# Optimization experiments

Measured on AMD Instinct MI355X. Metric: run time of the kernel, lower is better.

## Reference

```python
import jax, jax.numpy as jnp
import numpy as np

B, D, H, O = 32, 128, 256, 10


def setup_inputs() -> dict:
    key = jax.random.key(0)
    ks = jax.random.split(key, 8)
    return {
        "t": jax.random.uniform(ks[0], (1,), dtype=jnp.float32),
        "state_batch": jax.random.normal(ks[1], (2 * B, D), dtype=jnp.float32),
        "x0": jax.random.normal(ks[2], (B, D), dtype=jnp.float32),
        "x1": jax.random.normal(ks[3], (B, D), dtype=jnp.float32),
        "W1": jax.random.normal(ks[4], (D, H), dtype=jnp.float32) / np.sqrt(D),
        "b1": jax.random.normal(ks[5], (H,), dtype=jnp.float32) * 0.01,
        "W2": jax.random.normal(ks[6], (H, O), dtype=jnp.float32) / np.sqrt(H),
        "b2": jax.random.normal(ks[7], (O,), dtype=jnp.float32) * 0.01,
    }


def reference(t, state_batch, x0, x1, W1, b1, W2, b2):
    b = x0.shape[0]
    deviation, dev_velocity = state_batch[:b], state_batch[b:]  # [B,D] each
    tt = t[0]
    window = 4.0 * tt * (1.0 - tt)
    # point on the perturbed path
    x = x0 + tt * (x1 - x0) + window * deviation  # [B,D]

    def f_single(xs):  # [D] -> [O]
        return jnp.tanh(xs @ W1 + b1) @ W2 + b2

    def G_single(xs):  # [D] -> [D,D] pullback metric J^T J + eps I
        J = jax.jacrev(f_single)(xs)  # [O,D] (O small -> reverse mode)
        return J.T @ J + 1e-4 * jnp.eye(xs.shape[0], dtype=xs.dtype)

    # dG[b,i,j,k] = d G_ij / d x_k  -- replaces the torch double autograd loop
    dG = jax.vmap(jax.jacfwd(G_single))(x)  # [B,D,D,D]
    dG = dG / (jnp.sqrt(jnp.sum(dG * dG, axis=(1, 2, 3), keepdims=True)) + 1e-6)
    # Christoffel symbols (first kind, up to normalization as in source)
    Gamma = 0.5 * (dG + jnp.transpose(dG, (0, 2, 1, 3)) - jnp.transpose(dG, (0, 3, 1, 2)))
    a = -jnp.einsum('bijk,bj,bk->bi', Gamma, dev_velocity, dev_velocity)
    a = a / (jnp.linalg.norm(dev_velocity, axis=1, keepdims=True) + 1e-6)
    restoration = -0.1 * deviation
    return jnp.concatenate([dev_velocity, a + restoration], axis=0)  # [2B,D]
```

## Files before the change

kernel.cpp:

```cpp
#include <hip/hip_runtime.h>
#include <hip/hip_bf16.h>


#define NB 32

#define OP    0
#define OE    65536
#define OCW   163840
#define OAUN  245760
#define OVN   249856

template<int BF> __device__ __forceinline__ float ld(const void* p, int i) {
  if constexpr (BF) return __bfloat162float(((const __hip_bfloat16*)p)[i]);
  else return ((const float*)p)[i];
}
template<int BF> __device__ __forceinline__ void st(void* p, int i, float v) {
  if constexpr (BF) ((__hip_bfloat16*)p)[i] = __float2bfloat16(v);
  else ((float*)p)[i] = v;
}

__device__ __forceinline__ int blocksniff(const void* sb, int* sh) {
  if (threadIdx.x == 0) *sh = 0;
  __syncthreads();
  float v = fabsf(__bfloat162float(((const __hip_bfloat16*)sb)[threadIdx.x & 255]));
  if (!(v < 1000.0f)) atomicOr(sh, 1);
  __syncthreads();
  return (*sh == 0) ? 1 : 0;
}

#define LXS   0
#define LVS   128
#define LW2   256
#define LTMP  2816
#define LYS   3072
#define LSMV  3088
#define LSAR  3344
#define LF1   3600
#define LEL   5136
#define LCL   8208
#define LSW2  8320
#define LTOT  11392

template<int BF>
__device__ void k1_body(const void* tin, const void* sbin, const void* x0in,
                        const void* x1in, const void* W1in, const void* b1in,
                        const void* W2in, float* ws, float* sm) {
  int bid = blockIdx.x, t = threadIdx.x;
  if (bid < 256) {
    float* colh = sm;
    if (t < 128) colh[t] = ld<BF>(W1in, t * 256 + bid);
    __syncthreads();
    float pacc = 0.f;
    for (int d = 0; d < 128; d += 4) {
      float4 c4 = *(const float4*)&colh[d];
      pacc += c4.x * ld<BF>(W1in, (d + 0) * 256 + t);
      pacc += c4.y * ld<BF>(W1in, (d + 1) * 256 + t);
      pacc += c4.z * ld<BF>(W1in, (d + 2) * 256 + t);
      pacc += c4.w * ld<BF>(W1in, (d + 3) * 256 + t);
    }
    ws[OP + bid * 256 + t] = pacc;
    return;
  }
  int b = bid - 256;
  float tt = ld<BF>(tin, 0);
  float window = 4.f * tt * (1.f - tt);
  if (t < 128) {
    float dev = ld<BF>(sbin, b * 128 + t);
    float v   = ld<BF>(sbin, (NB + b) * 128 + t);
    float x0v = ld<BF>(x0in, b * 128 + t);
    float x1v = ld<BF>(x1in, b * 128 + t);
    sm[LXS + t] = x0v + tt * (x1v - x0v) + window * dev;
    sm[LVS + t] = v;
  }
  for (int i = t; i < 2560; i += 256) sm[LW2 + i] = ld<BF>(W2in, i);
  __syncthreads();
  float hacc = ld<BF>(b1in, t), wacc = 0.f;
  for (int d = 0; d < 128; ++d) {
    float w1v = ld<BF>(W1in, d * 256 + t);
    hacc += w1v * sm[LXS + d];
    wacc += w1v * sm[LVS + d];
  }
  float z  = tanhf(hacc);
  float sg = 1.f - z * z;
  float ug = -2.f * z * sg;
  sm[LSAR + t] = sg;
  sm[LTMP + t] = (t < 128) ? sm[LVS + t] * sm[LVS + t] : 0.f;
  __syncthreads();
  for (int off = 128; off > 0; off >>= 1) {
    if (t < off) sm[LTMP + t] += sm[LTMP + t + off];
    __syncthreads();
  }
  if (t == 0) ws[OVN + b] = sqrtf(sm[LTMP]);
  __syncthreads();
  sm[LTMP + t] = ug * wacc * wacc;
  __syncthreads();
  if (t < 10) {
    float y = 0.f;
    for (int h = 0; h < 256; ++h) y += sm[LW2 + h * 10 + t] * sm[LTMP + h];
    sm[LYS + t] = y;
  }
  __syncthreads();
  {
    float mg = 0.f;
    #pragma unroll
    for (int o = 0; o < 10; ++o) mg += sm[LW2 + t * 10 + o] * sm[LYS + o];
    sm[LSMV + t] = sg * mg;
  }
  for (int i = t; i < 3072; i += 256) {
    int g = i / 12, c = i % 12;
    sm[LSW2 + i] = (c < 10) ? sm[LSAR + g] * sm[LW2 + g * 10 + c] : 0.f;
  }
  __syncthreads();
  if (t < 128) {
    float a = 0.f;
    for (int g = 0; g < 256; ++g) a += ld<BF>(W1in, t * 256 + g) * sm[LSMV + g];
    ws[OAUN + b * 128 + t] = a;
  }
  if (t < 128) {
    float fa[10];
    #pragma unroll
    for (int o = 0; o < 10; ++o) fa[o] = 0.f;
    for (int g = 0; g < 256; ++g) {
      float w1v = ld<BF>(W1in, t * 256 + g);
      const float* sp = &sm[LSW2 + g * 12];
      float4 a0 = *(const float4*)sp;
      float4 a1 = *(const float4*)(sp + 4);
      float2 a2 = *(const float2*)(sp + 8);
      fa[0] += w1v * a0.x; fa[1] += w1v * a0.y; fa[2] += w1v * a0.z; fa[3] += w1v * a0.w;
      fa[4] += w1v * a1.x; fa[5] += w1v * a1.y; fa[6] += w1v * a1.z; fa[7] += w1v * a1.w;
      fa[8] += w1v * a2.x; fa[9] += w1v * a2.y;
    }
    #pragma unroll
    for (int o = 0; o < 10; ++o) sm[LF1 + t * 12 + o] = fa[o];
    sm[LF1 + t * 12 + 10] = 0.f; sm[LF1 + t * 12 + 11] = 0.f;
  }
  __syncthreads();
  float er[10];
  #pragma unroll
  for (int o = 0; o < 10; ++o) er[o] = 0.f;
  for (int d = 0; d < 128; ++d) {
    float w1v = ld<BF>(W1in, d * 256 + t);
    const float* fp = &sm[LF1 + d * 12];
    float4 a0 = *(const float4*)fp;
    float4 a1 = *(const float4*)(fp + 4);
    float2 a2 = *(const float2*)(fp + 8);
    er[0] += w1v * a0.x; er[1] += w1v * a0.y; er[2] += w1v * a0.z; er[3] += w1v * a0.w;
    er[4] += w1v * a1.x; er[5] += w1v * a1.y; er[6] += w1v * a1.z; er[7] += w1v * a1.w;
    er[8] += w1v * a2.x; er[9] += w1v * a2.y;
  }
  #pragma unroll
  for (int o = 0; o < 10; ++o) sm[LEL + t * 12 + o] = er[o];
  {
    float* gp = ws + OE + (b * 256 + t) * 12;
    *(float4*)gp       = make_float4(er[0], er[1], er[2], er[3]);
    *(float4*)(gp + 4) = make_float4(er[4], er[5], er[6], er[7]);
    *(float4*)(gp + 8) = make_float4(er[8], er[9], ug, 0.f);
  }
  __syncthreads();
  if (t < 100) {
    int o = t / 10, p = t % 10;
    float c = 0.f;
    for (int g = 0; g < 256; ++g)
      c += sm[LW2 + g * 10 + o] * sm[LSAR + g] * sm[LEL + g * 12 + p];
    sm[LCL + t] = c;
  }
  __syncthreads();
  {
    float w2r[10];
    #pragma unroll
    for (int p = 0; p < 10; ++p) w2r[p] = sm[LW2 + t * 10 + p];
    #pragma unroll
    for (int o = 0; o < 10; ++o) {
      float cw = 0.f;
      #pragma unroll
      for (int p = 0; p < 10; ++p) cw += sm[LCL + o * 10 + p] * w2r[p];
      ws[OCW + b * 2560 + o * 256 + t] = cw;
    }
  }
}

__global__ __launch_bounds__(256) void K1(const void* tin, const void* sbin,
                                          const void* x0in, const void* x1in,
                                          const void* W1in, const void* b1in,
                                          const void* W2in, float* ws) {
  __shared__ int sh;
  __shared__ __align__(16) float sm[LTOT];
  int bf = blocksniff(sbin, &sh);
  if (bf) k1_body<1>(tin, sbin, x0in, x1in, W1in, b1in, W2in, ws, sm);
  else    k1_body<0>(tin, sbin, x0in, x1in, W1in, b1in, W2in, ws, sm);
}

template<int BF>
__device__ void k2_body(const void* sbin, const void* W2in, void* out, float* ws,
                        float* rec, float* w2h, float* red) {
  int b = blockIdx.x, t = threadIdx.x;
  int w = t >> 6;
  for (int i = t; i < 3072; i += 256) rec[i] = ws[OE + b * 3072 + i];
  for (int i = t; i < 3072; i += 256) {
    int r = i / 12, c = i % 12;
    w2h[i] = (c < 10) ? ld<BF>(W2in, r * 10 + c) : 0.f;
  }
  __syncthreads();
  float cwr[10], er[10], w2r[10];
  #pragma unroll
  for (int o = 0; o < 10; ++o) cwr[o] = ws[OCW + b * 2560 + o * 256 + t];
  #pragma unroll
  for (int o = 0; o < 10; ++o) er[o] = rec[t * 12 + o];
  float uT = rec[t * 12 + 10];
  #pragma unroll
  for (int o = 0; o < 10; ++o) w2r[o] = w2h[t * 12 + o];
  float acc = 0.f;
  for (int i = 0; i < 64; ++i) {
    int h = w * 64 + i;
    float Ph = ws[OP + h * 256 + t];
    const float* rp = &rec[h * 12];
    float4 E0 = *(const float4*)rp;
    float4 E1 = *(const float4*)(rp + 4);
    float4 E2 = *(const float4*)(rp + 8);
    const float* wp = &w2h[h * 12];
    float4 W0 = *(const float4*)wp;
    float4 W1v = *(const float4*)(wp + 4);
    float4 W2v = *(const float4*)(wp + 8);
    float R = E0.x*w2r[0] + E0.y*w2r[1] + E0.z*w2r[2] + E0.w*w2r[3]
            + E1.x*w2r[4] + E1.y*w2r[5] + E1.z*w2r[6] + E1.w*w2r[7]
            + E2.x*w2r[8] + E2.y*w2r[9];
    float Rt = W0.x*er[0] + W0.y*er[1] + W0.z*er[2] + W0.w*er[3]
             + W1v.x*er[4] + W1v.y*er[5] + W1v.z*er[6] + W1v.w*er[7]
             + W2v.x*er[8] + W2v.y*er[9];
    float Qd = W0.x*cwr[0] + W0.y*cwr[1] + W0.z*cwr[2] + W0.w*cwr[3]
             + W1v.x*cwr[4] + W1v.y*cwr[5] + W1v.z*cwr[6] + W1v.w*cwr[7]
             + W2v.x*cwr[8] + W2v.y*cwr[9];
    acc += E2.z * Ph * (Ph * Qd + R * Rt);
  }
  red[t] = acc * uT;
  __syncthreads();
  for (int off = 128; off > 0; off >>= 1) {
    if (t < off) red[t] += red[t + off];
    __syncthreads();
  }
  float F = sqrtf(fmaxf(2.f * red[0], 0.f));
  float denom = (F + 1e-6f) * (ws[OVN + b] + 1e-6f);
  if (t < 128) {
    st<BF>(out, b * 128 + t, ld<BF>(sbin, (NB + b) * 128 + t));
    float dev = ld<BF>(sbin, b * 128 + t);
    float val = -ws[OAUN + b * 128 + t] / denom - 0.1f * dev;
    st<BF>(out, (NB + b) * 128 + t, val);
  }
}

__global__ __launch_bounds__(256) void K2(const void* sbin, const void* W2in,
                                          void* out, float* ws) {
  __shared__ int sh;
  __shared__ __align__(16) float rec[3072];
  __shared__ __align__(16) float w2h[3072];
  __shared__ float red[256];
  int bf = blocksniff(sbin, &sh);
  if (bf) k2_body<1>(sbin, W2in, out, ws, rec, w2h, red);
  else    k2_body<0>(sbin, W2in, out, ws, rec, w2h, red);
}

extern "C" void kernel_launch(void* const* d_in, const int* in_sizes, int n_in,
                              void* d_out, int out_size, void* d_ws, size_t ws_size,
                              hipStream_t stream) {
  float* ws = (float*)d_ws;
  const void* tin  = d_in[0];
  const void* sbin = d_in[1];
  const void* x0in = d_in[2];
  const void* x1in = d_in[3];
  const void* W1in = d_in[4];
  const void* b1in = d_in[5];
  const void* W2in = d_in[6];

  K1<<<dim3(288), dim3(256), 0, stream>>>(tin, sbin, x0in, x1in, W1in, b1in, W2in, ws);
  K2<<<dim3(32),  dim3(256), 0, stream>>>(sbin, W2in, d_out, ws);
}
```

Before: 113.4 us.

## Restructure K1/K2 reductions with wave shuffles and split F1 across all threads

The per-batch blocks in K1 now run first, ahead of the P-matrix blocks. The ys and vnorm reductions use wave shuffles instead of shared-memory tree reductions. The a_un matvec is derived algebraically from F1 and ys rather than a separate 256-long dot per thread, and the F1 and C computations are split across both thread halves with vectorized W1 loads. K2 uses float4 copies, batches P loads eight at a time, and replaces its tree reduction with a shuffle reduction. The aim is to cut serial reduction depth, barrier count and redundant W1 reads, at the cost of a slightly different floating-point summation order.

```diff
diff --git a/kernel.cpp b/kernel.cpp
--- a/kernel.cpp
+++ b/kernel.cpp
@@ -18,6 +18,17 @@
   if constexpr (BF) ((__hip_bfloat16*)p)[i] = __float2bfloat16(v);
   else ((float*)p)[i] = v;
 }
+__device__ __forceinline__ float b2f(unsigned short u) {
+  return __uint_as_float(((unsigned int)u) << 16);
+}
+template<int BF> __device__ __forceinline__ float4 ld4(const void* p, int i) {
+  if constexpr (BF) {
+    ushort4 u = *(const ushort4*)((const unsigned short*)p + i);
+    return make_float4(b2f(u.x), b2f(u.y), b2f(u.z), b2f(u.w));
+  } else {
+    return *(const float4*)((const float*)p + i);
+  }
+}
 
 __device__ __forceinline__ int blocksniff(const void* sb, int* sh) {
   if (threadIdx.x == 0) *sh = 0;
@@ -31,24 +42,34 @@
 #define LXS   0
 #define LVS   128
 #define LW2   256
-#define LTMP  2816
-#define LYS   3072
-#define LSMV  3088
-#define LSAR  3344
-#define LF1   3600
-#define LEL   5136
-#define LCL   8208
-#define LSW2  8320
-#define LTOT  11392
+#define LYS   2816
+#define LRED  2832
+#define LF1   2880
+#define LEL   4416
+#define LSW2  7488
+#define LCL   10560
+#define LCL2  10660
+#define LTOT  10760
+
+#define F1ACC(wv, gidx) do { \
+    const float* sp_ = &sm[LSW2 + (gidx)*12]; \
+    float4 s0_ = *(const float4*)sp_; \
+    float4 s1_ = *(const float4*)(sp_+4); \
+    float2 s2_ = *(const float2*)(sp_+8); \
+    fa[0]+=(wv)*s0_.x; fa[1]+=(wv)*s0_.y; fa[2]+=(wv)*s0_.z; fa[3]+=(wv)*s0_.w; \
+    fa[4]+=(wv)*s1_.x; fa[5]+=(wv)*s1_.y; fa[6]+=(wv)*s1_.z; fa[7]+=(wv)*s1_.w; \
+    fa[8]+=(wv)*s2_.x; fa[9]+=(wv)*s2_.y; \
+  } while (0)
 
 template<int BF>
 __device__ void k1_body(const void* tin, const void* sbin, const void* x0in,
                         const void* x1in, const void* W1in, const void* b1in,
                         const void* W2in, float* ws, float* sm) {
   int bid = blockIdx.x, t = threadIdx.x;
-  if (bid < 256) {
+  if (bid >= NB) {
+    int row = bid - NB;
     float* colh = sm;
-    if (t < 128) colh[t] = ld<BF>(W1in, t * 256 + bid);
+    if (t < 128) colh[t] = ld<BF>(W1in, t * 256 + row);
     __syncthreads();
     float pacc = 0.f;
     for (int d = 0; d < 128; d += 4) {
@@ -58,10 +79,11 @@
       pacc += c4.z * ld<BF>(W1in, (d + 2) * 256 + t);
       pacc += c4.w * ld<BF>(W1in, (d + 3) * 256 + t);
     }
-    ws[OP + bid * 256 + t] = pacc;
+    ws[OP + row * 256 + t] = pacc;
     return;
   }
-  int b = bid - 256;
+  int b = bid;
+  int w = t >> 6;
   float tt = ld<BF>(tin, 0);
   float window = 4.f * tt * (1.f - tt);
   if (t < 128) {
@@ -75,64 +97,71 @@
   for (int i = t; i < 2560; i += 256) sm[LW2 + i] = ld<BF>(W2in, i);
   __syncthreads();
   float hacc = ld<BF>(b1in, t), wacc = 0.f;
-  for (int d = 0; d < 128; ++d) {
-    float w1v = ld<BF>(W1in, d * 256 + t);
-    hacc += w1v * sm[LXS + d];
-    wacc += w1v * sm[LVS + d];
+  for (int d = 0; d < 128; d += 4) {
+    float4 xv = *(const float4*)&sm[LXS + d];
+    float4 vv = *(const float4*)&sm[LVS + d];
+    float w0 = ld<BF>(W1in, (d + 0) * 256 + t);
+    float w1 = ld<BF>(W1in, (d + 1) * 256 + t);
+    float w2 = ld<BF>(W1in, (d + 2) * 256 + t);
+    float w3 = ld<BF>(W1in, (d + 3) * 256 + t);
+    hacc += w0 * xv.x + w1 * xv.y + w2 * xv.z + w3 * xv.w;
+    wacc += w0 * vv.x + w1 * vv.y + w2 * vv.z + w3 * vv.w;
   }
   float z  = tanhf(hacc);
   float sg = 1.f - z * z;
   float ug = -2.f * z * sg;
-  sm[LSAR + t] = sg;
-  sm[LTMP + t] = (t < 128) ? sm[LVS + t] * sm[LVS + t] : 0.f;
-  __syncthreads();
-  for (int off = 128; off > 0; off >>= 1) {
-    if (t < off) sm[LTMP + t] += sm[LTMP + t + off];
-    __syncthreads();
-  }
-  if (t == 0) ws[OVN + b] = sqrtf(sm[LTMP]);
-  __syncthreads();
-  sm[LTMP + t] = ug * wacc * wacc;
-  __syncthreads();
-  if (t < 10) {
-    float y = 0.f;
-    for (int h = 0; h < 256; ++h) y += sm[LW2 + h * 10 + t] * sm[LTMP + h];
-    sm[LYS + t] = y;
-  }
-  __syncthreads();
+  float w2r[10];
+  #pragma unroll
+  for (int o = 0; o < 10; ++o) w2r[o] = sm[LW2 + t * 10 + o];
+  #pragma unroll
+  for (int o = 0; o < 10; ++o) sm[LSW2 + t * 12 + o] = sg * w2r[o];
+  float cval = ug * wacc * wacc;
+  float rv[11];
+  #pragma unroll
+  for (int o = 0; o < 10; ++o) rv[o] = cval * w2r[o];
+  rv[10] = (t < 128) ? sm[LVS + t] * sm[LVS + t] : 0.f;
+  #pragma unroll
+  for (int o = 0; o < 11; ++o) {
+    float v = rv[o];
+    #pragma unroll
+    for (int m = 32; m > 0; m >>= 1) v += __shfl_xor(v, m);
+    if ((t & 63) == 0) sm[LRED + w * 12 + o] = v;
+  }
+  __syncthreads();
+  if (t < 11) {
+    float s = sm[LRED + t] + sm[LRED + 12 + t] + sm[LRED + 24 + t] + sm[LRED + 36 + t];
+    if (t < 10) sm[LYS + t] = s;
+    else        ws[OVN + b] = sqrtf(s);
+  }
+  int half = t >> 7, r = t & 127;
+  float fa[10];
+  #pragma unroll
+  for (int o = 0; o < 10; ++o) fa[o] = 0.f;
   {
-    float mg = 0.f;
-    #pragma unroll
-    for (int o = 0; o < 10; ++o) mg += sm[LW2 + t * 10 + o] * sm[LYS + o];
-    sm[LSMV + t] = sg * mg;
-  }
-  for (int i = t; i < 3072; i += 256) {
-    int g = i / 12, c = i % 12;
-    sm[LSW2 + i] = (c < 10) ? sm[LSAR + g] * sm[LW2 + g * 10 + c] : 0.f;
-  }
-  __syncthreads();
-  if (t < 128) {
-    float a = 0.f;
-    for (int g = 0; g < 256; ++g) a += ld<BF>(W1in, t * 256 + g) * sm[LSMV + g];
-    ws[OAUN + b * 128 + t] = a;
-  }
-  if (t < 128) {
-    float fa[10];
-    #pragma unroll
-    for (int o = 0; o < 10; ++o) fa[o] = 0.f;
-    for (int g = 0; g < 256; ++g) {
-      float w1v = ld<BF>(W1in, t * 256 + g);
-      const float* sp = &sm[LSW2 + g * 12];
-      float4 a0 = *(const float4*)sp;
-      float4 a1 = *(const float4*)(sp + 4);
-      float2 a2 = *(const float2*)(sp + 8);
-      fa[0] += w1v * a0.x; fa[1] += w1v * a0.y; fa[2] += w1v * a0.z; fa[3] += w1v * a0.w;
-      fa[4] += w1v * a1.x; fa[5] += w1v * a1.y; fa[6] += w1v * a1.z; fa[7] += w1v * a1.w;
-      fa[8] += w1v * a2.x; fa[9] += w1v * a2.y;
+    const int gbase = half * 128;
+    for (int gg = 0; gg < 128; gg += 4) {
+      int g = gbase + gg;
+      float4 w4 = ld4<BF>(W1in, r * 256 + g);
+      F1ACC(w4.x, g + 0);
+      F1ACC(w4.y, g + 1);
+      F1ACC(w4.z, g + 2);
+      F1ACC(w4.w, g + 3);
     }
-    #pragma unroll
-    for (int o = 0; o < 10; ++o) sm[LF1 + t * 12 + o] = fa[o];
-    sm[LF1 + t * 12 + 10] = 0.f; sm[LF1 + t * 12 + 11] = 0.f;
+  }
+  if (half) {
+    #pragma unroll
+    for (int o = 0; o < 10; ++o) sm[LF1 + r * 12 + o] = fa[o];
+  }
+  __syncthreads();
+  if (!half) {
+    float aun = 0.f;
+    #pragma unroll
+    for (int o = 0; o < 10; ++o) {
+      float f = fa[o] + sm[LF1 + r * 12 + o];
+      sm[LF1 + r * 12 + o] = f;
+      aun += f * sm[LYS + o];
+    }
+    ws[OAUN + b * 128 + t] = aun;
   }
   __syncthreads();
   float er[10];
@@ -157,25 +186,26 @@
     *(float4*)(gp + 8) = make_float4(er[8], er[9], ug, 0.f);
   }
   __syncthreads();
-  if (t < 100) {
-    int o = t / 10, p = t % 10;
-    float c = 0.f;
-    for (int g = 0; g < 256; ++g)
-      c += sm[LW2 + g * 10 + o] * sm[LSAR + g] * sm[LEL + g * 12 + p];
-    sm[LCL + t] = c;
-  }
-  __syncthreads();
-  {
-    float w2r[10];
-    #pragma unroll
-    for (int p = 0; p < 10; ++p) w2r[p] = sm[LW2 + t * 10 + p];
-    #pragma unroll
-    for (int o = 0; o < 10; ++o) {
-      float cw = 0.f;
-      #pragma unroll
-      for (int p = 0; p < 10; ++p) cw += sm[LCL + o * 10 + p] * w2r[p];
-      ws[OCW + b * 2560 + o * 256 + t] = cw;
-    }
+  float cpart = 0.f;
+  if (t < 200) {
+    int gh = (t >= 100) ? 1 : 0;
+    int idx = t - gh * 100;
+    int o = idx / 10, p = idx - o * 10;
+    const float* sa = &sm[LSW2 + gh * 1536 + o];
+    const float* sb = &sm[LEL  + gh * 1536 + p];
+    #pragma unroll 4
+    for (int g = 0; g < 128; ++g) cpart += sa[g * 12] * sb[g * 12];
+    if (gh) sm[LCL2 + idx] = cpart;
+  }
+  __syncthreads();
+  if (t < 100) sm[LCL + t] = cpart + sm[LCL2 + t];
+  __syncthreads();
+  #pragma unroll
+  for (int o = 0; o < 10; ++o) {
+    float cw = 0.f;
+    #pragma unroll
+    for (int p = 0; p < 10; ++p) cw += sm[LCL + o * 10 + p] * w2r[p];
+    ws[OCW + b * 2560 + o * 256 + t] = cw;
   }
 }
 
@@ -195,50 +225,69 @@
                         float* rec, float* w2h, float* red) {
   int b = blockIdx.x, t = threadIdx.x;
   int w = t >> 6;
-  for (int i = t; i < 3072; i += 256) rec[i] = ws[OE + b * 3072 + i];
+  {
+    float4* rec4 = (float4*)rec;
+    const float4* src = (const float4*)(ws + OE + b * 3072);
+    for (int i = t; i < 768; i += 256) rec4[i] = src[i];
+  }
   for (int i = t; i < 3072; i += 256) {
-    int r = i / 12, c = i % 12;
+    int r = i / 12, c = i - r * 12;
     w2h[i] = (c < 10) ? ld<BF>(W2in, r * 10 + c) : 0.f;
   }
   __syncthreads();
   float cwr[10], er[10], w2r[10];
   #pragma unroll
   for (int o = 0; o < 10; ++o) cwr[o] = ws[OCW + b * 2560 + o * 256 + t];
-  #pragma unroll
-  for (int o = 0; o < 10; ++o) er[o] = rec[t * 12 + o];
-  float uT = rec[t * 12 + 10];
-  #pragma unroll
-  for (int o = 0; o < 10; ++o) w2r[o] = w2h[t * 12 + o];
+  float uT;
+  {
+    float4 e0 = *(const float4*)&rec[t * 12];
+    float4 e1 = *(const float4*)&rec[t * 12 + 4];
+    float4 e2 = *(const float4*)&rec[t * 12 + 8];
+    er[0]=e0.x; er[1]=e0.y; er[2]=e0.z; er[3]=e0.w;
+    er[4]=e1.x; er[5]=e1.y; er[6]=e1.z; er[7]=e1.w;
+    er[8]=e2.x; er[9]=e2.y; uT = e2.z;
+    float4 p0 = *(const float4*)&w2h[t * 12];
+    float4 p1 = *(const float4*)&w2h[t * 12 + 4];
+    float2 p2 = *(const float2*)&w2h[t * 12 + 8];
+    w2r[0]=p0.x; w2r[1]=p0.y; w2r[2]=p0.z; w2r[3]=p0.w;
+    w2r[4]=p1.x; w2r[5]=p1.y; w2r[6]=p1.z; w2r[7]=p1.w;
+    w2r[8]=p2.x; w2r[9]=p2.y;
+  }
   float acc = 0.f;
-  for (int i = 0; i < 64; ++i) {
-    int h = w * 64 + i;
-    float Ph = ws[OP + h * 256 + t];
-    const float* rp = &rec[h * 12];
-    float4 E0 = *(const float4*)rp;
-    float4 E1 = *(const float4*)(rp + 4);
-    float4 E2 = *(const float4*)(rp + 8);
-    const float* wp = &w2h[h * 12];
-    float4 W0 = *(const float4*)wp;
-    float4 W1v = *(const float4*)(wp + 4);
-    float4 W2v = *(const float4*)(wp + 8);
-    float R = E0.x*w2r[0] + E0.y*w2r[1] + E0.z*w2r[2] + E0.w*w2r[3]
-            + E1.x*w2r[4] + E1.y*w2r[5] + E1.z*w2r[6] + E1.w*w2r[7]
-            + E2.x*w2r[8] + E2.y*w2r[9];
-    float Rt = W0.x*er[0] + W0.y*er[1] + W0.z*er[2] + W0.w*er[3]
-             + W1v.x*er[4] + W1v.y*er[5] + W1v.z*er[6] + W1v.w*er[7]
-             + W2v.x*er[8] + W2v.y*er[9];
-    float Qd = W0.x*cwr[0] + W0.y*cwr[1] + W0.z*cwr[2] + W0.w*cwr[3]
-             + W1v.x*cwr[4] + W1v.y*cwr[5] + W1v.z*cwr[6] + W1v.w*cwr[7]
-             + W2v.x*cwr[8] + W2v.y*cwr[9];
-    acc += E2.z * Ph * (Ph * Qd + R * Rt);
-  }
-  red[t] = acc * uT;
-  __syncthreads();
-  for (int off = 128; off > 0; off >>= 1) {
-    if (t < off) red[t] += red[t + off];
-    __syncthreads();
-  }
-  float F = sqrtf(fmaxf(2.f * red[0], 0.f));
+  for (int i0 = 0; i0 < 64; i0 += 8) {
+    float ph[8];
+    #pragma unroll
+    for (int j = 0; j < 8; ++j)
+      ph[j] = ws[OP + (w * 64 + i0 + j) * 256 + t];
+    #pragma unroll
+    for (int j = 0; j < 8; ++j) {
+      int h = w * 64 + i0 + j;
+      const float* rp = &rec[h * 12];
+      float4 E0 = *(const float4*)rp;
+      float4 E1 = *(const float4*)(rp + 4);
+      float4 E2 = *(const float4*)(rp + 8);
+      const float* wp = &w2h[h * 12];
+      float4 W0 = *(const float4*)wp;
+      float4 W1v = *(const float4*)(wp + 4);
+      float4 W2v = *(const float4*)(wp + 8);
+      float R = E0.x*w2r[0] + E0.y*w2r[1] + E0.z*w2r[2] + E0.w*w2r[3]
+              + E1.x*w2r[4] + E1.y*w2r[5] + E1.z*w2r[6] + E1.w*w2r[7]
+              + E2.x*w2r[8] + E2.y*w2r[9];
+      float Rt = W0.x*er[0] + W0.y*er[1] + W0.z*er[2] + W0.w*er[3]
+               + W1v.x*er[4] + W1v.y*er[5] + W1v.z*er[6] + W1v.w*er[7]
+               + W2v.x*er[8] + W2v.y*er[9];
+      float Qd = W0.x*cwr[0] + W0.y*cwr[1] + W0.z*cwr[2] + W0.w*cwr[3]
+               + W1v.x*cwr[4] + W1v.y*cwr[5] + W1v.z*cwr[6] + W1v.w*cwr[7]
+               + W2v.x*cwr[8] + W2v.y*cwr[9];
+      acc += E2.z * ph[j] * (ph[j] * Qd + R * Rt);
+    }
+  }
+  acc *= uT;
+  #pragma unroll
+  for (int m = 32; m > 0; m >>= 1) acc += __shfl_xor(acc, m);
+  if ((t & 63) == 0) red[w] = acc;
+  __syncthreads();
+  float F = sqrtf(fmaxf(2.f * (red[0] + red[1] + red[2] + red[3]), 0.f));
   float denom = (F + 1e-6f) * (ws[OVN + b] + 1e-6f);
   if (t < 128) {
     st<BF>(out, b * 128 + t, ld<BF>(sbin, (NB + b) * 128 + t));
@@ -253,7 +302,7 @@
   __shared__ int sh;
   __shared__ __align__(16) float rec[3072];
   __shared__ __align__(16) float w2h[3072];
-  __shared__ float red[256];
+  __shared__ float red[4];
   int bf = blocksniff(sbin, &sh);
   if (bf) k2_body<1>(sbin, W2in, out, ws, rec, w2h, red);
   else    k2_body<0>(sbin, W2in, out, ws, rec, w2h, red);
```

Measured after the change: 102.3 us. 9.8% less time.
